# Kernel tuning notes

Measured on AMD Instinct MI355X. Metric: run time of the kernel, lower is better.

The kernel has to match this reference:

```python
import jax, jax.numpy as jnp
import numpy as np
from jax import lax

BT, ST, NT = 32, 8, 1024
CH = [128, 64, 32, 16, 8]
DIL = [1, 2, 4, 8, 16]
K = 5
EPS = 1e-5


def setup_inputs() -> dict:
    key = jax.random.key(0)
    ks = jax.random.split(key, 32)
    inp = {}
    inp["x"] = jax.random.normal(ks[0], (BT, ST, CH[0], NT), jnp.float32)
    nt_out = NT * 32  # 5 x2 upsamples
    inp["targets"] = jax.random.uniform(ks[1], (BT, 3, nt_out, ST), dtype=jnp.float32)
    for i in range(4):
        inp[f"w{i}"] = jax.random.normal(ks[2 + i], (CH[i + 1], CH[i], K), jnp.float32) * 0.05
        inp[f"g{i}"] = 1.0 + 0.1 * jax.random.normal(ks[6 + i], (CH[i + 1],), jnp.float32)
        inp[f"b{i}"] = 0.1 * jax.random.normal(ks[10 + i], (CH[i + 1],), jnp.float32)
        inp[f"m{i}"] = 0.1 * jax.random.normal(ks[14 + i], (CH[i + 1],), jnp.float32)
        inp[f"v{i}"] = 0.5 + 0.5 * jax.random.uniform(ks[18 + i], (CH[i + 1],), dtype=jnp.float32)
    inp["w_out"] = jax.random.normal(ks[22], (3, CH[4], K), jnp.float32) * 0.05
    inp["b_out"] = jax.random.normal(ks[23], (3,), jnp.float32) * 0.05
    return inp


def _conv(x, w, d):
    # reflect-padded dilated conv1d, same length out (torch padding_mode='reflect')
    p = ((K - 1) * d + 1) // 2
    xp = jnp.pad(x, ((0, 0), (0, 0), (p, p)), mode="reflect")
    return lax.conv_general_dilated(xp, w, window_strides=(1,), padding="VALID",
                                    rhs_dilation=(d,),
                                    dimension_numbers=("NCH", "OIH", "NCH"))


def _up2(x):
    # F.interpolate(scale_factor=2, mode='linear', align_corners=False)
    L = x.shape[-1]
    coords = (jnp.arange(2 * L, dtype=jnp.float32) + 0.5) / 2.0 - 0.5
    coords = jnp.clip(coords, 0.0, L - 1.0)
    i0 = jnp.floor(coords).astype(jnp.int32)
    i1 = jnp.minimum(i0 + 1, L - 1)
    w = coords - i0.astype(jnp.float32)
    return x[..., i0] * (1.0 - w) + x[..., i1] * w


def _forward(x, targets, ws, gs, bs, ms, vs, w_out, b_out):
    h = x.reshape(BT * ST, CH[0], NT)
    for i in range(4):
        h = _conv(h, ws[i], DIL[i])
        inv = gs[i] / jnp.sqrt(vs[i] + EPS)
        h = h * inv[None, :, None] + (bs[i] - ms[i] * inv)[None, :, None]  # eval-mode BN
        h = jax.nn.relu(h)
        h = _up2(h)
    h = _conv(h, w_out, DIL[4]) + b_out[None, :, None]
    h = _up2(h)
    out = h.reshape(BT, ST, 3, h.shape[-1]).transpose(0, 2, 3, 1)  # [bt, 3, nt_out, st]
    # vectorized equivalent of the per-(i,j) Python loop counting non-all-zero targets
    mask = jnp.any(targets != 0, axis=(1, 2))  # [bt, st]
    num = jnp.sum(mask).astype(jnp.float32)
    loss = jnp.sum(-targets * jax.nn.log_softmax(out, axis=1)) / (num * targets.shape[2])
    return out, loss


def reference(x, targets, w0, w1, w2, w3, g0, g1, g2, g3, b0, b1, b2, b3,
              m0, m1, m2, m3, v0, v1, v2, v3, w_out, b_out):
    return _forward(x, targets, [w0, w1, w2, w3], [g0, g1, g2, g3],
                    [b0, b1, b2, b3], [m0, m1, m2, m3], [v0, v1, v2, v3],
                    w_out, b_out)
```

## Files before the change

kernel.cpp:

```cpp
#include <hip/hip_runtime.h>
#include <hip/hip_bf16.h>
#include <cstdint>
#include <cstddef>

#define K5 5
#define BNEPS 1e-5f

typedef __attribute__((ext_vector_type(8))) short short8v;
typedef __attribute__((ext_vector_type(4))) short short4v;
typedef __attribute__((ext_vector_type(4))) float float4v;

struct __attribute__((packed, aligned(4))) f4u { float4v v; };

__device__ inline float bf2f(short s) {
    __hip_bfloat16 h = *(__hip_bfloat16*)&s;
    return __bfloat162float(h);
}
__device__ inline short f2bf(float f) {
    __hip_bfloat16 h = __float2bfloat16(f);
    return *(short*)&h;
}

template<int CIN, int COUT, int MROWS, int KPAD>
__device__ inline void wprep_body(const float* __restrict__ w,
                                  short* __restrict__ wb, int blk, int tid) {
    int idx = blk * 256 + tid;
    if (idx >= MROWS * KPAD) return;
    int co = idx / KPAD, kk = idx - co * KPAD;
    int tap = kk / CIN, ci = kk & (CIN - 1);
    float v = (co < COUT && tap < K5) ? w[((size_t)co * CIN + ci) * K5 + tap] : 0.f;
    wb[idx] = f2bf(v);
}

__global__ __launch_bounds__(256) void wprep_all_ker(
    const float* __restrict__ w0, const float* __restrict__ w1,
    const float* __restrict__ w2, const float* __restrict__ w3,
    const float* __restrict__ w4,
    short* __restrict__ wb0, short* __restrict__ wb1, short* __restrict__ wb2,
    short* __restrict__ wb3, short* __restrict__ wb4) {
    int b = blockIdx.x, t = threadIdx.x;
    if (b < 160)      wprep_body<128, 64, 64, 640>(w0, wb0, b, t);
    else if (b < 200) wprep_body<64, 32, 32, 320>(w1, wb1, b - 160, t);
    else if (b < 210) wprep_body<32, 16, 16, 160>(w2, wb2, b - 200, t);
    else if (b < 216) wprep_body<16, 8, 16, 96>(w3, wb3, b - 210, t);
    else              wprep_body<8, 3, 16, 64>(w4, wb4, b - 216, t);
}

template<int CIN, int COUT, int DIL, int LOUT, int T_TILE, int WT, int WCO,
         bool HAS_BN, int IN_MODE, int OUT_MODE>
__global__ __launch_bounds__(256) void conv_ker(
    const void* __restrict__ in_, const short* __restrict__ wb,
    const float* __restrict__ gg, const float* __restrict__ bb,
    const float* __restrict__ mm, const float* __restrict__ vv,
    void* __restrict__ out_)
{
    constexpr int P = 2 * DIL;
    constexpr int XT = T_TILE + 4 * DIL;
    constexpr int ROWW = (CIN == 8) ? 24 : (CIN + 8);
    constexpr int K = CIN * K5;
    constexpr int KPAD = ((K + 31) / 32) * 32;
    constexpr int NSTEP = KPAD / 32;
    constexpr int MT = (COUT + 15) / 16;
    constexpr int CT = MT / WCO;
    constexpr int TN = T_TILE / (16 * WT);
    constexpr int LIN = LOUT;
    constexpr int LIN_BASE = (IN_MODE == 1) ? (LOUT / 2) : LOUT;
    static_assert(WT * WCO == 4, "4 waves");
    static_assert(MT % WCO == 0, "co split");
    static_assert(T_TILE % (16 * WT) == 0, "tile split");

    __shared__ short sx[XT * ROWW];
    __shared__ float ssc[COUT], ssh[COUT];

    const int n = blockIdx.x;
    const int t0 = blockIdx.y * T_TILE;
    const int tid = threadIdx.x;

    if (tid < COUT) {
        if constexpr (HAS_BN) {
            float inv = gg[tid] * rsqrtf(vv[tid] + BNEPS);
            ssc[tid] = inv;
            ssh[tid] = bb[tid] - mm[tid] * inv;
        } else {
            ssc[tid] = 1.f;
            ssh[tid] = bb[tid];
        }
    }

    if constexpr (IN_MODE == 0) {
        static_assert(XT % 4 == 0, "XT mult of 4");
        constexpr int T4 = XT / 4;
        constexpr int NITEM = T4 * (CIN / 8);
        const float* in = (const float*)in_;
        for (int uidx = tid; uidx < NITEM; uidx += 256) {
            int t4 = uidx % T4;
            int ci0 = (uidx / T4) * 8;
            const int u0 = t0 - P + 4 * t4;
            const float* base = in + ((size_t)n * CIN + ci0) * LIN_BASE;
            short8v rows[4];
            bool fast = (u0 >= 0) && (u0 + 3 <= LIN - 1);
            if (fast) {
#pragma unroll
                for (int j = 0; j < 8; ++j) {
                    f4u xv = *(const f4u*)(base + (size_t)j * LIN_BASE + u0);
#pragma unroll
                    for (int r = 0; r < 4; ++r) rows[r][j] = f2bf(xv.v[r]);
                }
            } else {
#pragma unroll
                for (int r = 0; r < 4; ++r) {
                    int u = u0 + r;
                    u = (u < 0) ? -u : u;
                    u = (u >= LIN) ? (2 * (LIN - 1) - u) : u;
#pragma unroll
                    for (int j = 0; j < 8; ++j)
                        rows[r][j] = f2bf(base[(size_t)j * LIN_BASE + u]);
                }
            }
            short* dst = sx + (4 * t4) * ROWW + ci0;
            *(short8v*)(dst) = rows[0];
            *(short8v*)(dst + ROWW) = rows[1];
            *(short8v*)(dst + 2 * ROWW) = rows[2];
            *(short8v*)(dst + 3 * ROWW) = rows[3];
        }
    } else {
        constexpr int CPR = CIN / 8;
        const short* inb = (const short*)in_ + (size_t)n * LIN_BASE * CIN;
        for (int uidx = tid; uidx < XT * CPR; uidx += 256) {
            int ci0 = (uidx % CPR) * 8;
            int t = uidx / CPR;
            int u = t0 - P + t;
            u = (u < 0) ? -u : u;
            u = (u >= LIN) ? (2 * (LIN - 1) - u) : u;
            int i = u >> 1;
            int ia, ib; float wa, wbw;
            if (u & 1) { ia = i; ib = (i + 1 < LIN_BASE) ? i + 1 : LIN_BASE - 1; wa = 0.75f; wbw = 0.25f; }
            else if (i == 0) { ia = 0; ib = 0; wa = 1.0f; wbw = 0.0f; }
            else { ia = i - 1; ib = i; wa = 0.25f; wbw = 0.75f; }
            short8v va = *(const short8v*)(inb + (size_t)ia * CIN + ci0);
            short8v vb = *(const short8v*)(inb + (size_t)ib * CIN + ci0);
            short8v pack;
#pragma unroll
            for (int j = 0; j < 8; ++j) {
                short sa = va[j], sb = vb[j];
                pack[j] = f2bf(wa * bf2f(sa) + wbw * bf2f(sb));
            }
            *(short8v*)(sx + t * ROWW + ci0) = pack;
        }
    }
    __syncthreads();

    const int wvi = tid >> 6;
    const int lane = tid & 63;
    const int ln = lane & 15;
    const int q = lane >> 4;
    const int tg = wvi % WT;
    const int cg = wvi / WT;
    const int tw = tg * (TN * 16);

    float4v acc[CT][TN];
#pragma unroll
    for (int c = 0; c < CT; ++c)
#pragma unroll
        for (int j = 0; j < TN; ++j)
            acc[c][j] = (float4v){0.f, 0.f, 0.f, 0.f};

    const short* arow[CT];
#pragma unroll
    for (int c = 0; c < CT; ++c)
        arow[c] = wb + ((size_t)((cg * CT + c) * 16 + ln)) * KPAD + q * 8;

    if constexpr (NSTEP <= 6) {
        short8v aall[NSTEP][CT];
#pragma unroll
        for (int s = 0; s < NSTEP; ++s)
#pragma unroll
            for (int c = 0; c < CT; ++c)
                aall[s][c] = *(const short8v*)(arow[c] + s * 32);
#pragma unroll
        for (int s = 0; s < NSTEP; ++s) {
            const int kk = s * 32 + q * 8;
            int tap = kk / CIN;
            const int ci0 = kk & (CIN - 1);
            if constexpr (KPAD != K) {
                tap = (tap < K5) ? tap : (K5 - 1);
            }
            short8v b[TN];
#pragma unroll
            for (int j = 0; j < TN; ++j)
                b[j] = *(const short8v*)(sx + (tw + j * 16 + ln + tap * DIL) * ROWW + ci0);
            if constexpr (KPAD != K) {
                if (kk >= K) {
                    short8v z = {0, 0, 0, 0, 0, 0, 0, 0};
#pragma unroll
                    for (int j = 0; j < TN; ++j) b[j] = z;
                }
            }
#pragma unroll
            for (int c = 0; c < CT; ++c)
#pragma unroll
                for (int j = 0; j < TN; ++j)
                    acc[c][j] = __builtin_amdgcn_mfma_f32_16x16x32_bf16(aall[s][c], b[j], acc[c][j], 0, 0, 0);
        }
    } else {
        short8v a0[CT], a1[CT], a2[CT];
#pragma unroll
        for (int c = 0; c < CT; ++c) a0[c] = *(const short8v*)(arow[c]);
#pragma unroll
        for (int c = 0; c < CT; ++c) a1[c] = *(const short8v*)(arow[c] + 32);
#pragma unroll 1
        for (int s = 0; s < NSTEP; ++s) {
            if (s + 2 < NSTEP) {
#pragma unroll
                for (int c = 0; c < CT; ++c)
                    a2[c] = *(const short8v*)(arow[c] + (s + 2) * 32);
            }
            const int kk = s * 32 + q * 8;
            int tap = kk / CIN;
            const int ci0 = kk & (CIN - 1);
            if constexpr (KPAD != K) {
                tap = (tap < K5) ? tap : (K5 - 1);
            }
            short8v b[TN];
#pragma unroll
            for (int j = 0; j < TN; ++j)
                b[j] = *(const short8v*)(sx + (tw + j * 16 + ln + tap * DIL) * ROWW + ci0);
            if constexpr (KPAD != K) {
                if (kk >= K) {
                    short8v z = {0, 0, 0, 0, 0, 0, 0, 0};
#pragma unroll
                    for (int j = 0; j < TN; ++j) b[j] = z;
                }
            }
#pragma unroll
            for (int c = 0; c < CT; ++c)
#pragma unroll
                for (int j = 0; j < TN; ++j)
                    acc[c][j] = __builtin_amdgcn_mfma_f32_16x16x32_bf16(a0[c], b[j], acc[c][j], 0, 0, 0);
#pragma unroll
            for (int c = 0; c < CT; ++c) { a0[c] = a1[c]; a1[c] = a2[c]; }
        }
    }

    if constexpr (OUT_MODE == 0) {
        short* ob = (short*)out_ + ((size_t)n * LOUT + t0 + tw) * COUT;
#pragma unroll
        for (int c = 0; c < CT; ++c)
#pragma unroll
            for (int j = 0; j < TN; ++j) {
                if ((COUT % 16 == 0) || (q * 4 + 3 < COUT)) {
                    float4v v = acc[c][j];
                    short4v pk;
#pragma unroll
                    for (int r = 0; r < 4; ++r) {
                        int co = (cg * CT + c) * 16 + q * 4 + r;
                        float val = v[r] * ssc[co] + ssh[co];
                        if constexpr (HAS_BN) val = fmaxf(val, 0.f);
                        pk[r] = f2bf(val);
                    }
                    *(short4v*)(ob + (size_t)(j * 16 + ln) * COUT + (cg * CT + c) * 16 + q * 4) = pk;
                }
            }
    } else {
        float* ob = (float*)out_ + (size_t)n * COUT * LOUT + t0 + tw + ln;
#pragma unroll
        for (int c = 0; c < CT; ++c)
#pragma unroll
            for (int j = 0; j < TN; ++j) {
                float4v v = acc[c][j];
#pragma unroll
                for (int r = 0; r < 4; ++r) {
                    int co = (cg * CT + c) * 16 + q * 4 + r;
                    if ((COUT % 16 == 0) || co < COUT) {
                        float val = v[r] * ssc[co] + ssh[co];
                        if constexpr (HAS_BN) val = fmaxf(val, 0.f);
                        ob[(size_t)co * LOUT + j * 16] = val;
                    }
                }
            }
    }
}

__global__ __launch_bounds__(256) void up_loss_ker(
    const float* __restrict__ h4, const float* __restrict__ targets,
    float* __restrict__ out, float* __restrict__ loss_sum, int* __restrict__ flags)
{
    constexpr int L = 16384, LO = 32768;
    const int bt = blockIdx.x;
    const int t0 = blockIdx.y * 256;
    const int tid = threadIdx.x;
    const int i0 = t0 >> 1;

    __shared__ float sh[3 * 8 * 132];
    __shared__ int snz[8];
    __shared__ float swv[4];

    {
        const bool interior = (i0 >= 1) && (i0 + 130 <= L - 1);
        for (int idx = tid; idx < 24 * 33; idx += 256) {
            int row = idx / 33;
            int qd = idx - row * 33;
            int c = row >> 3, s = row & 7;
            int nn = bt * 8 + s;
            const float* src = h4 + ((size_t)nn * 3 + c) * L;
            int bi0 = i0 - 1 + 4 * qd;
            float4v v;
            if (interior) {
                v = ((const f4u*)(src + bi0))->v;
            } else {
#pragma unroll
                for (int k = 0; k < 4; ++k) {
                    int bi = bi0 + k;
                    bi = bi < 0 ? 0 : (bi > L - 1 ? L - 1 : bi);
                    v[k] = src[bi];
                }
            }
            *(float4v*)(sh + row * 132 + 4 * qd) = v;
        }
    }
    if (tid < 8) snz[tid] = 0;
    __syncthreads();

    const int tl = tid >> 1;
    const int st4 = (tid & 1) * 4;

    float lsum = 0.f;
    int nzm = 0;
#pragma unroll
    for (int rr = 0; rr < 2; ++rr) {
        int t = t0 + rr * 128 + tl;
        int li = (t >> 1) - i0 + 1;
        float o[3][4];
#pragma unroll
        for (int c = 0; c < 3; ++c)
#pragma unroll
            for (int s = 0; s < 4; ++s) {
                const float* row = sh + ((c << 3) + st4 + s) * 132;
                float v;
                if (t & 1) v = 0.75f * row[li] + 0.25f * row[li + 1];
                else       v = 0.25f * row[li - 1] + 0.75f * row[li];
                o[c][s] = v;
            }
        float tg[3][4];
#pragma unroll
        for (int c = 0; c < 3; ++c) {
            size_t obase = (((size_t)bt * 3 + c) * LO + t) * 8 + st4;
            float4v ov = { o[c][0], o[c][1], o[c][2], o[c][3] };
            *(float4v*)(out + obase) = ov;
            float4v tv = *(const float4v*)(targets + obase);
            tg[c][0] = tv[0]; tg[c][1] = tv[1]; tg[c][2] = tv[2]; tg[c][3] = tv[3];
        }
#pragma unroll
        for (int s = 0; s < 4; ++s) {
            float a0 = o[0][s], a1 = o[1][s], a2 = o[2][s];
            float mx = fmaxf(a0, fmaxf(a1, a2));
            float e0 = __expf(a0 - mx), e1 = __expf(a1 - mx), e2 = __expf(a2 - mx);
            float lse = mx + __logf(e0 + e1 + e2);
            lsum += tg[0][s] * (lse - a0) + tg[1][s] * (lse - a1) + tg[2][s] * (lse - a2);
            if ((tg[0][s] != 0.f) | (tg[1][s] != 0.f) | (tg[2][s] != 0.f)) nzm |= 1 << s;
        }
    }
    if (nzm) {
#pragma unroll
        for (int s = 0; s < 4; ++s) if (nzm & (1 << s)) snz[st4 + s] = 1;
    }

#pragma unroll
    for (int off = 32; off > 0; off >>= 1) lsum += __shfl_down(lsum, off, 64);
    if ((tid & 63) == 0) swv[tid >> 6] = lsum;
    __syncthreads();
    if (tid == 0) atomicAdd(loss_sum, swv[0] + swv[1] + swv[2] + swv[3]);
    if (tid < 8 && snz[tid]) atomicOr(&flags[bt * 8 + tid], 1);
}

__global__ __launch_bounds__(256) void finalize_ker(
    const int* __restrict__ flags, const float* __restrict__ loss_sum,
    float* __restrict__ out_loss)
{
    __shared__ int s[256];
    s[threadIdx.x] = flags[threadIdx.x] ? 1 : 0;
    __syncthreads();
    for (int off = 128; off > 0; off >>= 1) {
        if (threadIdx.x < off) s[threadIdx.x] += s[threadIdx.x + off];
        __syncthreads();
    }
    if (threadIdx.x == 0) out_loss[0] = loss_sum[0] / ((float)s[0] * 32768.0f);
}

extern "C" void kernel_launch(void* const* d_in, const int* in_sizes, int n_in,
                              void* d_out, int out_size, void* d_ws, size_t ws_size,
                              hipStream_t stream)
{
    const float* x  = (const float*)d_in[0];
    const float* tg = (const float*)d_in[1];
    const float* w0 = (const float*)d_in[2];
    const float* g0 = (const float*)d_in[3];
    const float* b0 = (const float*)d_in[4];
    const float* m0 = (const float*)d_in[5];
    const float* v0 = (const float*)d_in[6];
    const float* w1 = (const float*)d_in[7];
    const float* g1 = (const float*)d_in[8];
    const float* b1 = (const float*)d_in[9];
    const float* m1 = (const float*)d_in[10];
    const float* v1 = (const float*)d_in[11];
    const float* w2 = (const float*)d_in[12];
    const float* g2 = (const float*)d_in[13];
    const float* b2 = (const float*)d_in[14];
    const float* m2 = (const float*)d_in[15];
    const float* v2 = (const float*)d_in[16];
    const float* w3 = (const float*)d_in[17];
    const float* g3 = (const float*)d_in[18];
    const float* b3 = (const float*)d_in[19];
    const float* m3 = (const float*)d_in[20];
    const float* v3 = (const float*)d_in[21];
    const float* w_out = (const float*)d_in[22];
    const float* b_out = (const float*)d_in[23];
    float* outp = (float*)d_out;

    char* ws = (char*)d_ws;
    int* flags = (int*)ws;
    float* loss_sum = (float*)(ws + 1024);
    short* wb0 = (short*)(ws + 4096);
    short* wb1 = (short*)(ws + 86016);
    short* wb2 = (short*)(ws + 106496);
    short* wb3 = (short*)(ws + 111616);
    short* wb4 = (short*)(ws + 114688);
    const size_t BUF_OFF = 131072;
    const size_t BUFN = (size_t)16777216;
    float* bufA = (float*)(ws + BUF_OFF);
    float* bufB = (ws_size >= BUF_OFF + 2 * BUFN * 4)
                      ? (bufA + BUFN)
                      : (float*)d_out;

    hipMemsetAsync(d_ws, 0, 4096, stream);

    wprep_all_ker<<<220, 256, 0, stream>>>(w0, w1, w2, w3, w_out,
                                           wb0, wb1, wb2, wb3, wb4);

    conv_ker<128, 64, 1, 1024, 128, 2, 2, true, 0, 0>
        <<<dim3(256, 8), 256, 0, stream>>>(x, wb0, g0, b0, m0, v0, bufA);
    conv_ker<64, 32, 2, 2048, 256, 2, 2, true, 1, 0>
        <<<dim3(256, 8), 256, 0, stream>>>(bufA, wb1, g1, b1, m1, v1, bufB);
    conv_ker<32, 16, 4, 4096, 512, 4, 1, true, 1, 0>
        <<<dim3(256, 8), 256, 0, stream>>>(bufB, wb2, g2, b2, m2, v2, bufA);
    conv_ker<16, 8, 8, 8192, 512, 4, 1, true, 1, 0>
        <<<dim3(256, 16), 256, 0, stream>>>(bufA, wb3, g3, b3, m3, v3, bufB);
    conv_ker<8, 3, 16, 16384, 512, 4, 1, false, 1, 1>
        <<<dim3(256, 32), 256, 0, stream>>>(bufB, wb4, b_out, b_out, b_out, b_out, bufA);
    up_loss_ker<<<dim3(32, 128), 256, 0, stream>>>(bufA, tg, outp, loss_sum, flags);
    finalize_ker<<<1, 256, 0, stream>>>(flags, loss_sum, outp + (size_t)(out_size - 1));
}
```

Before: 511.0 us.

## Swizzle conv LDS tiles, batch global loads, and prefetch targets in loss kernel

Applies an XOR swizzle to the shared-memory input tile of the conv kernels so MFMA operand reads from LDS spread across banks. The staging loops are restructured to issue several independent global loads before converting and storing them, raising memory-level parallelism. The loss kernel loads its target tiles at kernel start, before the shared-memory fill and barrier, so that latency overlaps with the h4 staging. The cost is higher register pressure from the batched loads and some extra index arithmetic.

```diff
diff --git a/kernel.cpp b/kernel.cpp
--- a/kernel.cpp
+++ b/kernel.cpp
@@ -57,6 +57,7 @@
     constexpr int P = 2 * DIL;
     constexpr int XT = T_TILE + 4 * DIL;
     constexpr int ROWW = (CIN == 8) ? 24 : (CIN + 8);
+    constexpr int CPR = CIN / 8;
     constexpr int K = CIN * K5;
     constexpr int KPAD = ((K + 31) / 32) * 32;
     constexpr int NSTEP = KPAD / 32;
@@ -76,6 +77,11 @@
     const int t0 = blockIdx.y * T_TILE;
     const int tid = threadIdx.x;
 
+    auto swzoff = [](int row, int c) -> int {
+        int pc = c ^ ((row >> 2) & (CPR - 1));
+        return row * ROWW + (pc << 3);
+    };
+
     if (tid < COUT) {
         if constexpr (HAS_BN) {
             float inv = gg[tid] * rsqrtf(vv[tid] + BNEPS);
@@ -90,62 +96,94 @@
     if constexpr (IN_MODE == 0) {
         static_assert(XT % 4 == 0, "XT mult of 4");
         constexpr int T4 = XT / 4;
-        constexpr int NITEM = T4 * (CIN / 8);
+        constexpr int NITEM = T4 * CPR;
+        constexpr int U0 = 2;
         const float* in = (const float*)in_;
-        for (int uidx = tid; uidx < NITEM; uidx += 256) {
-            int t4 = uidx % T4;
-            int ci0 = (uidx / T4) * 8;
-            const int u0 = t0 - P + 4 * t4;
-            const float* base = in + ((size_t)n * CIN + ci0) * LIN_BASE;
-            short8v rows[4];
-            bool fast = (u0 >= 0) && (u0 + 3 <= LIN - 1);
-            if (fast) {
-#pragma unroll
-                for (int j = 0; j < 8; ++j) {
-                    f4u xv = *(const f4u*)(base + (size_t)j * LIN_BASE + u0);
-#pragma unroll
-                    for (int r = 0; r < 4; ++r) rows[r][j] = f2bf(xv.v[r]);
+        for (int base = tid; base < NITEM; base += 256 * U0) {
+            f4u xv[U0][8];
+            int t4s[U0], ci0s[U0], u0s[U0];
+            bool fasts[U0], vals[U0];
+#pragma unroll
+            for (int u = 0; u < U0; ++u) {
+                int idx = base + u * 256;
+                vals[u] = idx < NITEM;
+                int id2 = vals[u] ? idx : 0;
+                int t4 = id2 % T4;
+                int ci0 = (id2 / T4) * 8;
+                int u0 = t0 - P + 4 * t4;
+                bool fast = (u0 >= 0) && (u0 + 3 <= LIN - 1);
+                int uc = u0 < 0 ? 0 : (u0 > LIN - 4 ? LIN - 4 : u0);
+                const float* basep = in + ((size_t)n * CIN + ci0) * LIN_BASE;
+#pragma unroll
+                for (int j = 0; j < 8; ++j)
+                    xv[u][j] = *(const f4u*)(basep + (size_t)j * LIN_BASE + uc);
+                t4s[u] = t4; ci0s[u] = ci0; u0s[u] = u0; fasts[u] = fast;
+            }
+#pragma unroll
+            for (int u = 0; u < U0; ++u) {
+                if (!vals[u]) continue;
+                short8v rows[4];
+                if (fasts[u]) {
+#pragma unroll
+                    for (int j = 0; j < 8; ++j)
+#pragma unroll
+                        for (int r = 0; r < 4; ++r)
+                            rows[r][j] = f2bf(xv[u][j].v[r]);
+                } else {
+                    const float* basep = in + ((size_t)n * CIN + ci0s[u]) * LIN_BASE;
+#pragma unroll
+                    for (int r = 0; r < 4; ++r) {
+                        int uu = u0s[u] + r;
+                        uu = (uu < 0) ? -uu : uu;
+                        uu = (uu >= LIN) ? (2 * (LIN - 1) - uu) : uu;
+#pragma unroll
+                        for (int j = 0; j < 8; ++j)
+                            rows[r][j] = f2bf(basep[(size_t)j * LIN_BASE + uu]);
+                    }
                 }
-            } else {
-#pragma unroll
-                for (int r = 0; r < 4; ++r) {
-                    int u = u0 + r;
-                    u = (u < 0) ? -u : u;
-                    u = (u >= LIN) ? (2 * (LIN - 1) - u) : u;
-#pragma unroll
-                    for (int j = 0; j < 8; ++j)
-                        rows[r][j] = f2bf(base[(size_t)j * LIN_BASE + u]);
-                }
-            }
-            short* dst = sx + (4 * t4) * ROWW + ci0;
-            *(short8v*)(dst) = rows[0];
-            *(short8v*)(dst + ROWW) = rows[1];
-            *(short8v*)(dst + 2 * ROWW) = rows[2];
-            *(short8v*)(dst + 3 * ROWW) = rows[3];
+                int cc = ci0s[u] >> 3;
+#pragma unroll
+                for (int r = 0; r < 4; ++r)
+                    *(short8v*)(sx + swzoff(4 * t4s[u] + r, cc)) = rows[r];
+            }
         }
     } else {
-        constexpr int CPR = CIN / 8;
+        constexpr int ITEMS = XT * CPR;
+        constexpr int UU = 4;
         const short* inb = (const short*)in_ + (size_t)n * LIN_BASE * CIN;
-        for (int uidx = tid; uidx < XT * CPR; uidx += 256) {
-            int ci0 = (uidx % CPR) * 8;
-            int t = uidx / CPR;
-            int u = t0 - P + t;
-            u = (u < 0) ? -u : u;
-            u = (u >= LIN) ? (2 * (LIN - 1) - u) : u;
-            int i = u >> 1;
-            int ia, ib; float wa, wbw;
-            if (u & 1) { ia = i; ib = (i + 1 < LIN_BASE) ? i + 1 : LIN_BASE - 1; wa = 0.75f; wbw = 0.25f; }
-            else if (i == 0) { ia = 0; ib = 0; wa = 1.0f; wbw = 0.0f; }
-            else { ia = i - 1; ib = i; wa = 0.25f; wbw = 0.75f; }
-            short8v va = *(const short8v*)(inb + (size_t)ia * CIN + ci0);
-            short8v vb = *(const short8v*)(inb + (size_t)ib * CIN + ci0);
-            short8v pack;
-#pragma unroll
-            for (int j = 0; j < 8; ++j) {
-                short sa = va[j], sb = vb[j];
-                pack[j] = f2bf(wa * bf2f(sa) + wbw * bf2f(sb));
-            }
-            *(short8v*)(sx + t * ROWW + ci0) = pack;
+        for (int base = tid; base < ITEMS; base += 256 * UU) {
+            short8v va[UU], vb[UU];
+            float wav[UU], wbv[UU];
+            int trow[UU], cc[UU];
+            bool vals[UU];
+#pragma unroll
+            for (int u = 0; u < UU; ++u) {
+                int idx = base + u * 256;
+                vals[u] = idx < ITEMS;
+                int id2 = vals[u] ? idx : 0;
+                int ci0 = (id2 % CPR) * 8;
+                int t = id2 / CPR;
+                int uu2 = t0 - P + t;
+                uu2 = (uu2 < 0) ? -uu2 : uu2;
+                uu2 = (uu2 >= LIN) ? (2 * (LIN - 1) - uu2) : uu2;
+                int i = uu2 >> 1;
+                int ia, ib; float wa, wbw;
+                if (uu2 & 1) { ia = i; ib = (i + 1 < LIN_BASE) ? i + 1 : LIN_BASE - 1; wa = 0.75f; wbw = 0.25f; }
+                else if (i == 0) { ia = 0; ib = 0; wa = 1.0f; wbw = 0.0f; }
+                else { ia = i - 1; ib = i; wa = 0.25f; wbw = 0.75f; }
+                va[u] = *(const short8v*)(inb + (size_t)ia * CIN + ci0);
+                vb[u] = *(const short8v*)(inb + (size_t)ib * CIN + ci0);
+                wav[u] = wa; wbv[u] = wbw; trow[u] = t; cc[u] = ci0 >> 3;
+            }
+#pragma unroll
+            for (int u = 0; u < UU; ++u) {
+                if (!vals[u]) continue;
+                short8v pack;
+#pragma unroll
+                for (int j = 0; j < 8; ++j)
+                    pack[j] = f2bf(wav[u] * bf2f(va[u][j]) + wbv[u] * bf2f(vb[u][j]));
+                *(short8v*)(sx + swzoff(trow[u], cc[u])) = pack;
+            }
         }
     }
     __syncthreads();
@@ -188,7 +226,7 @@
             short8v b[TN];
 #pragma unroll
             for (int j = 0; j < TN; ++j)
-                b[j] = *(const short8v*)(sx + (tw + j * 16 + ln + tap * DIL) * ROWW + ci0);
+                b[j] = *(const short8v*)(sx + swzoff(tw + j * 16 + ln + tap * DIL, ci0 >> 3));
             if constexpr (KPAD != K) {
                 if (kk >= K) {
                     short8v z = {0, 0, 0, 0, 0, 0, 0, 0};
@@ -224,7 +262,7 @@
             short8v b[TN];
 #pragma unroll
             for (int j = 0; j < TN; ++j)
-                b[j] = *(const short8v*)(sx + (tw + j * 16 + ln + tap * DIL) * ROWW + ci0);
+                b[j] = *(const short8v*)(sx + swzoff(tw + j * 16 + ln + tap * DIL, ci0 >> 3));
             if constexpr (KPAD != K) {
                 if (kk >= K) {
                     short8v z = {0, 0, 0, 0, 0, 0, 0, 0};
@@ -295,34 +333,59 @@
     __shared__ int snz[8];
     __shared__ float swv[4];
 
-    {
-        const bool interior = (i0 >= 1) && (i0 + 130 <= L - 1);
+    const int tl = tid >> 1;
+    const int st4 = (tid & 1) * 4;
+
+    float4v tgv[2][3];
+#pragma unroll
+    for (int rr = 0; rr < 2; ++rr) {
+        int t = t0 + rr * 128 + tl;
+#pragma unroll
+        for (int c = 0; c < 3; ++c) {
+            size_t obase = (((size_t)bt * 3 + c) * LO + t) * 8 + st4;
+            tgv[rr][c] = *(const float4v*)(targets + obase);
+        }
+    }
+
+    const bool interior = (i0 >= 1) && (i0 + 130 <= L - 1);
+    if (interior) {
+        for (int base = tid; base < 24 * 33; base += 1024) {
+            float4v vv[4]; int ro[4], qd[4]; bool val[4];
+#pragma unroll
+            for (int u = 0; u < 4; ++u) {
+                int idx = base + u * 256;
+                val[u] = idx < 24 * 33;
+                int id2 = val[u] ? idx : 0;
+                int row = id2 / 33;
+                int q = id2 - row * 33;
+                int c = row >> 3, s = row & 7;
+                const float* src = h4 + ((size_t)(bt * 8 + s) * 3 + c) * L;
+                vv[u] = ((const f4u*)(src + (i0 - 1 + 4 * q)))->v;
+                ro[u] = row; qd[u] = q;
+            }
+#pragma unroll
+            for (int u = 0; u < 4; ++u)
+                if (val[u]) *(float4v*)(sh + ro[u] * 132 + 4 * qd[u]) = vv[u];
+        }
+    } else {
         for (int idx = tid; idx < 24 * 33; idx += 256) {
             int row = idx / 33;
-            int qd = idx - row * 33;
+            int q = idx - row * 33;
             int c = row >> 3, s = row & 7;
-            int nn = bt * 8 + s;
-            const float* src = h4 + ((size_t)nn * 3 + c) * L;
-            int bi0 = i0 - 1 + 4 * qd;
+            const float* src = h4 + ((size_t)(bt * 8 + s) * 3 + c) * L;
+            int bi0 = i0 - 1 + 4 * q;
             float4v v;
-            if (interior) {
-                v = ((const f4u*)(src + bi0))->v;
-            } else {
-#pragma unroll
-                for (int k = 0; k < 4; ++k) {
-                    int bi = bi0 + k;
-                    bi = bi < 0 ? 0 : (bi > L - 1 ? L - 1 : bi);
-                    v[k] = src[bi];
-                }
-            }
-            *(float4v*)(sh + row * 132 + 4 * qd) = v;
+#pragma unroll
+            for (int k = 0; k < 4; ++k) {
+                int bi = bi0 + k;
+                bi = bi < 0 ? 0 : (bi > L - 1 ? L - 1 : bi);
+                v[k] = src[bi];
+            }
+            *(float4v*)(sh + row * 132 + 4 * q) = v;
         }
     }
     if (tid < 8) snz[tid] = 0;
     __syncthreads();
-
-    const int tl = tid >> 1;
-    const int st4 = (tid & 1) * 4;
 
     float lsum = 0.f;
     int nzm = 0;
@@ -341,14 +404,11 @@
                 else       v = 0.25f * row[li - 1] + 0.75f * row[li];
                 o[c][s] = v;
             }
-        float tg[3][4];
 #pragma unroll
         for (int c = 0; c < 3; ++c) {
             size_t obase = (((size_t)bt * 3 + c) * LO + t) * 8 + st4;
             float4v ov = { o[c][0], o[c][1], o[c][2], o[c][3] };
             *(float4v*)(out + obase) = ov;
-            float4v tv = *(const float4v*)(targets + obase);
-            tg[c][0] = tv[0]; tg[c][1] = tv[1]; tg[c][2] = tv[2]; tg[c][3] = tv[3];
         }
 #pragma unroll
         for (int s = 0; s < 4; ++s) {
@@ -356,8 +416,9 @@
             float mx = fmaxf(a0, fmaxf(a1, a2));
             float e0 = __expf(a0 - mx), e1 = __expf(a1 - mx), e2 = __expf(a2 - mx);
             float lse = mx + __logf(e0 + e1 + e2);
-            lsum += tg[0][s] * (lse - a0) + tg[1][s] * (lse - a1) + tg[2][s] * (lse - a2);
-            if ((tg[0][s] != 0.f) | (tg[1][s] != 0.f) | (tg[2][s] != 0.f)) nzm |= 1 << s;
+            float g0 = tgv[rr][0][s], g1 = tgv[rr][1][s], g2 = tgv[rr][2][s];
+            lsum += g0 * (lse - a0) + g1 * (lse - a1) + g2 * (lse - a2);
+            if ((g0 != 0.f) | (g1 != 0.f) | (g2 != 0.f)) nzm |= 1 << s;
         }
     }
     if (nzm) {
```

After: 505.8 us. About the same (-1.0%).
